# Kernel optimization log

Hardware: AMD Instinct MI355X
Metric: run time of the kernel (lower is better)

Reference implementation:

```python
import jax, jax.numpy as jnp
import numpy as np

B, SQ, SK = 2, 2048, 2048
D, H = 1024, 16
HD = D // H              # head_dim = 64
R = 128                  # rel_pos_max_distance
P = 2 * R + 1            # num_pos_ids = 257
RADIUS = 256             # local_attention_radius


def setup_inputs() -> dict:
    key = jax.random.key(0)
    ks = jax.random.split(key, 8)
    s = 0.02
    return {
        "Q": jax.random.normal(ks[0], (B, SQ, D), dtype=jnp.float32),
        "K": jax.random.normal(ks[1], (B, SK, D), dtype=jnp.float32),
        "V": jax.random.normal(ks[2], (B, SK, D), dtype=jnp.float32),
        "Wq": jax.random.normal(ks[3], (D, D), dtype=jnp.float32) * s,
        "Wk": jax.random.normal(ks[4], (D, D), dtype=jnp.float32) * s,
        "Wv": jax.random.normal(ks[5], (D, D), dtype=jnp.float32) * s,
        "Wo": jax.random.normal(ks[6], (D, D), dtype=jnp.float32) * s,
        "E": jax.random.normal(ks[7], (P, D), dtype=jnp.float32) * s,  # rel_embeds
    }


def _split_heads(x, W):
    # bias-free projection then split: B x S x D -> B x H x S x HD
    y = x @ W.T
    b, s, _ = y.shape
    return y.reshape(b, s, H, HD).transpose(0, 2, 1, 3)


def reference(Q, K, V, Wq, Wk, Wv, Wo, E):
    q = _split_heads(Q, Wq)  # B,H,Sq,HD
    k = _split_heads(K, Wk)  # B,H,Sk,HD
    v = _split_heads(V, Wv)  # B,H,Sk,HD

    # rel_embeds reshape matches torch: E[p] viewed as (head_dim, num_heads)
    rel = E.reshape(P, HD, H).transpose(2, 0, 1)           # H,P,HD
    Q_rel = jnp.einsum("bhqd,hpd->bhqp", q, rel)           # B,H,Sq,P

    # slided relative position ids: clip(j - i, -R, R) + R
    i = jnp.arange(SQ)[:, None]
    j = jnp.arange(SK)[None, :]
    rel_ids = jnp.clip(j - i, -R, R) + R                   # Sq,Sk
    rel_shift = jnp.take_along_axis(
        Q_rel, jnp.broadcast_to(rel_ids, (B, H, SQ, SK)), axis=3
    )                                                       # B,H,Sq,Sk

    energy = (jnp.einsum("bhqd,bhkd->bhqk", q, k) + rel_shift) / jnp.sqrt(
        jnp.float32(HD)
    )

    # local attention mask: True = masked (outside window of radius RADIUS)
    mask = jnp.abs(j - i) > RADIUS                          # Sq,Sk
    mask = mask & ~jnp.all(mask, axis=-1, keepdims=True)    # never mask full rows
    energy = jnp.where(mask[None, None], -jnp.inf, energy)

    attn = jax.nn.softmax(energy, axis=-1)                  # B,H,Sq,Sk
    out = jnp.einsum("bhqk,bhkd->bhqd", attn, v)            # B,H,Sq,HD
    # torch: view(B,H,Sq,HD).permute(0,2,3,1).flatten(2,3) -> B,Sq,(HD*H)
    out = out.transpose(0, 2, 3, 1).reshape(B, SQ, D)
    return out @ Wo.T
```

## Files before the change

kernel.cpp:

```cpp
#include <hip/hip_runtime.h>
#include <hip/hip_bf16.h>

#define BATCH 2
#define SQn 2048
#define SKn 2048
#define DMODEL 1024
#define NH 16
#define HD 64
#define NPOS 257
#define RWIN 128
#define RADIUS 256

typedef __attribute__((ext_vector_type(8))) short bf16x8;
typedef __attribute__((ext_vector_type(4))) float f32x4;

static __device__ __forceinline__ unsigned short f2bf(float f) {
    union { float f; unsigned u; } v; v.f = f;
    unsigned r = (v.u + 0x7FFFu + ((v.u >> 16) & 1u)) >> 16;
    return (unsigned short)r;
}
static __device__ __forceinline__ float bf2f(unsigned short b) {
    union { unsigned u; float f; } v; v.u = ((unsigned)b) << 16;
    return v.f;
}

static __device__ __forceinline__ void gl_lds16(const unsigned short* g, unsigned short* l) {
    __builtin_amdgcn_global_load_lds(
        (const __attribute__((address_space(1))) unsigned*)g,
        (__attribute__((address_space(3))) unsigned*)l, 16, 0, 0);
}

#define SWZ(row) (((row) ^ ((row) >> 2)) & 3)

__global__ __launch_bounds__(256) void convert_kernel(
    const float* __restrict__ Q, const float* __restrict__ K, const float* __restrict__ V,
    const float* __restrict__ Wq, const float* __restrict__ Wk, const float* __restrict__ Wv,
    const float* __restrict__ Wo,
    unsigned short* __restrict__ xb,
    unsigned short* __restrict__ wb,
    unsigned short* __restrict__ wob)
{
    int i = blockIdx.x * 256 + threadIdx.x;
    const float* src;
    unsigned short* dst;
    int off;
    if (i < 3145728) {
        int which = i >> 20;
        off = i & 1048575;
        src = which == 0 ? Q : (which == 1 ? K : V);
        dst = xb + (size_t)which * 4194304;
    } else {
        int i2 = i - 3145728;
        int which = i2 >> 18;
        off = i2 & 262143;
        src = which == 0 ? Wq : (which == 1 ? Wk : (which == 2 ? Wv : Wo));
        dst = which < 3 ? wb + (size_t)which * 1048576 : wob;
    }
    float4 v4 = ((const float4*)src)[off];
    ushort4 o4;
    o4.x = f2bf(v4.x); o4.y = f2bf(v4.y); o4.z = f2bf(v4.z); o4.w = f2bf(v4.w);
    ((ushort4*)dst)[off] = o4;
}

__global__ __launch_bounds__(256) void mfma_gemm(
    const unsigned short* __restrict__ Xall,
    const unsigned short* __restrict__ Wall,
    unsigned short* __restrict__ Yall)
{
    __shared__ unsigned short sA[128 * 32];
    __shared__ unsigned short sB[128 * 32];
    __shared__ unsigned short sT[64 * 136];

    const int tid  = threadIdx.x;
    const int wv   = tid >> 6;
    const int lane = tid & 63;
    const int quad = lane >> 4;
    const int l15  = lane & 15;
    const int z    = blockIdx.z;
    const int m0   = blockIdx.x * 128;
    const int n0   = blockIdx.y * 128;
    const int wr   = (wv >> 1) * 64;
    const int wc   = (wv & 1) * 64;

    const unsigned short* X = Xall + (size_t)z * (4096 * 1024);
    const unsigned short* W = Wall + (size_t)z * (1024 * 1024);

    int aoff[4], boff[4];
#pragma unroll
    for (int t = 0; t < 4; ++t) {
        int row = wr + t * 16 + l15;
        aoff[t] = row * 32 + ((quad ^ SWZ(row)) * 8);
        int col = wc + t * 16 + l15;
        boff[t] = col * 32 + ((quad ^ SWZ(col)) * 8);
    }

    int srow[2], scg[2], sf[2];
#pragma unroll
    for (int r = 0; r < 2; ++r) {
        int f = r * 256 + tid;
        sf[r] = f;
        srow[r] = f >> 2;
        scg[r] = (f & 3) ^ SWZ(srow[r]);
    }

    f32x4 acc[4][4];
#pragma unroll
    for (int i = 0; i < 4; ++i)
#pragma unroll
        for (int j = 0; j < 4; ++j)
            acc[i][j] = (f32x4){0.f, 0.f, 0.f, 0.f};

    for (int k0 = 0; k0 < 1024; k0 += 32) {
        __syncthreads();
#pragma unroll
        for (int r = 0; r < 2; ++r) {
            gl_lds16(X + (size_t)(m0 + srow[r]) * 1024 + k0 + scg[r] * 8, &sA[sf[r] * 8]);
            gl_lds16(W + (size_t)(n0 + srow[r]) * 1024 + k0 + scg[r] * 8, &sB[sf[r] * 8]);
        }
        __syncthreads();

        bf16x8 af[4], bfr[4];
#pragma unroll
        for (int t = 0; t < 4; ++t) af[t]  = *(const bf16x8*)&sA[aoff[t]];
#pragma unroll
        for (int t = 0; t < 4; ++t) bfr[t] = *(const bf16x8*)&sB[boff[t]];
#pragma unroll
        for (int i = 0; i < 4; ++i)
#pragma unroll
            for (int j = 0; j < 4; ++j)
                acc[i][j] = __builtin_amdgcn_mfma_f32_16x16x32_bf16(af[i], bfr[j], acc[i][j], 0, 0, 0);
    }

    unsigned short* Y = Yall + (size_t)z * (4096 * 1024);
    const int b_ = m0 >> 11;
    const int s0 = m0 & (SQn - 1);

    if (z < 2) {
#pragma unroll
        for (int i = 0; i < 4; ++i) {
            int mbase = s0 + wr + i * 16 + quad * 4;
#pragma unroll
            for (int j = 0; j < 4; ++j) {
                int col = n0 + wc + j * 16 + l15;
                int h = col >> 6, dd = col & 63;
                unsigned short* yb = Y + (((size_t)(b_ * NH + h) * SQn) << 6) + dd;
#pragma unroll
                for (int r = 0; r < 4; ++r)
                    yb[(size_t)(mbase + r) << 6] = f2bf(acc[i][j][r]);
            }
        }
    } else {
#pragma unroll
        for (int hh = 0; hh < 2; ++hh) {
            __syncthreads();
            if ((wv & 1) == hh) {
#pragma unroll
                for (int i = 0; i < 4; ++i) {
                    int mloc = wr + i * 16 + quad * 4;
#pragma unroll
                    for (int j = 0; j < 4; ++j) {
                        ushort4 pk;
                        pk.x = f2bf(acc[i][j][0]);
                        pk.y = f2bf(acc[i][j][1]);
                        pk.z = f2bf(acc[i][j][2]);
                        pk.w = f2bf(acc[i][j][3]);
                        *(ushort4*)&sT[(j * 16 + l15) * 136 + mloc] = pk;
                    }
                }
            }
            __syncthreads();
            int h = (n0 >> 6) + hh;
            unsigned short* yb = Y + ((size_t)(b_ * NH + h) * HD) * SKn + s0;
#pragma unroll
            for (int it = 0; it < 4; ++it) {
                int u = it * 256 + tid;
                int dd = u >> 4, mc = u & 15;
                uint4 val = *(const uint4*)&sT[dd * 136 + mc * 8];
                *(uint4*)(yb + (size_t)dd * SKn + mc * 8) = val;
            }
        }
    }
}

__global__ __launch_bounds__(256) void gemm_out(
    const unsigned short* __restrict__ X,
    const unsigned short* __restrict__ W,
    float* __restrict__ Y)
{
    __shared__ unsigned short sA[64 * 32];
    __shared__ unsigned short sB[128 * 32];

    const int tid  = threadIdx.x;
    const int wv   = tid >> 6;
    const int lane = tid & 63;
    const int quad = lane >> 4;
    const int l15  = lane & 15;
    const int m0   = blockIdx.x * 64;
    const int n0   = blockIdx.y * 128;
    const int wr   = (wv >> 1) * 32;
    const int wc   = (wv & 1) * 64;

    int aoff[2], boff[4];
#pragma unroll
    for (int i = 0; i < 2; ++i) {
        int row = wr + i * 16 + l15;
        aoff[i] = row * 32 + ((quad ^ SWZ(row)) * 8);
    }
#pragma unroll
    for (int j = 0; j < 4; ++j) {
        int col = wc + j * 16 + l15;
        boff[j] = col * 32 + ((quad ^ SWZ(col)) * 8);
    }

    const int af_  = tid;
    const int arow = af_ >> 2;
    const int acs  = (af_ & 3) ^ SWZ(arow);
    int bf_[2], brow[2], bcs[2];
#pragma unroll
    for (int r = 0; r < 2; ++r) {
        int f = r * 256 + tid;
        bf_[r] = f; brow[r] = f >> 2; bcs[r] = (f & 3) ^ SWZ(brow[r]);
    }

    f32x4 acc[2][4];
#pragma unroll
    for (int i = 0; i < 2; ++i)
#pragma unroll
        for (int j = 0; j < 4; ++j)
            acc[i][j] = (f32x4){0.f, 0.f, 0.f, 0.f};

    for (int k0 = 0; k0 < 1024; k0 += 32) {
        __syncthreads();
        gl_lds16(X + (size_t)(m0 + arow) * 1024 + k0 + acs * 8, &sA[af_ * 8]);
#pragma unroll
        for (int r = 0; r < 2; ++r)
            gl_lds16(W + (size_t)(n0 + brow[r]) * 1024 + k0 + bcs[r] * 8, &sB[bf_[r] * 8]);
        __syncthreads();

        bf16x8 af[2], bfr[4];
#pragma unroll
        for (int i = 0; i < 2; ++i) af[i]  = *(const bf16x8*)&sA[aoff[i]];
#pragma unroll
        for (int j = 0; j < 4; ++j) bfr[j] = *(const bf16x8*)&sB[boff[j]];
#pragma unroll
        for (int i = 0; i < 2; ++i)
#pragma unroll
            for (int j = 0; j < 4; ++j)
                acc[i][j] = __builtin_amdgcn_mfma_f32_16x16x32_bf16(af[i], bfr[j], acc[i][j], 0, 0, 0);
    }

#pragma unroll
    for (int i = 0; i < 2; ++i) {
        int mbase = m0 + wr + i * 16 + quad * 4;
#pragma unroll
        for (int j = 0; j < 4; ++j) {
            int col = n0 + wc + j * 16 + l15;
#pragma unroll
            for (int r = 0; r < 4; ++r)
                Y[(size_t)(mbase + r) * DMODEL + col] = acc[i][j][r];
        }
    }
}

__global__ __launch_bounds__(256) void relt_kernel(
    const float* __restrict__ E, unsigned short* __restrict__ relTb)
{
    int idx = blockIdx.x * 256 + threadIdx.x;
    const int total = NH * NPOS * HD;
    if (idx < total) {
        int d = idx & (HD - 1);
        int p = (idx >> 6) % NPOS;
        int h = idx / (NPOS * HD);
        relTb[idx] = f2bf(E[(size_t)p * DMODEL + d * NH + h]);
    }
}

#define BIAS_S 9.765625e-4f

__global__ __launch_bounds__(256) void attn_mfma(
    const unsigned short* __restrict__ q,
    const unsigned short* __restrict__ k,
    const unsigned short* __restrict__ vT,
    const unsigned short* __restrict__ relTb,
    unsigned short* __restrict__ aob)
{
    __shared__ unsigned short sQ[64 * 64];
    __shared__ unsigned short sK[64 * 64];
    __shared__ unsigned short sVt[64 * 64];
    __shared__ unsigned short sP[4][16 * 72];
    __shared__ signed char    sq8[64 * 260];

    const int tid  = threadIdx.x;
    const int w    = tid >> 6;
    const int lane = tid & 63;
    const int quad = lane >> 4;
    const int l15  = lane & 15;
    const int bh   = blockIdx.x >> 5;
    const int q0   = (blockIdx.x & 31) << 6;
    const int h    = bh & (NH - 1);
    const int b    = bh >> 4;

    {
        const unsigned short* gq = q + ((size_t)bh * SQn + q0) * HD;
#pragma unroll
        for (int r2 = 0; r2 < 2; ++r2) {
            int f = r2 * 256 + tid;
            int row = f >> 3, c = (f & 7) ^ (row & 7);
            gl_lds16(gq + row * HD + c * 8, &sQ[f * 8]);
        }
    }
    __syncthreads();

    const int qrow = w * 16 + l15;
    const int qs = (quad ^ (qrow & 7)) * 8;
    bf16x8 a0 = *(const bf16x8*)&sQ[qrow * 64 + qs];
    bf16x8 a1 = *(const bf16x8*)&sQ[qrow * 64 + (qs ^ 32)];

    const int myrow = w * 16 + quad * 4;
    for (int c5 = 0; c5 < 5; ++c5) {
        __syncthreads();
        const unsigned short* gr = relTb + ((size_t)h * NPOS + c5 * 64) * HD;
#pragma unroll
        for (int r2 = 0; r2 < 2; ++r2) {
            int f = r2 * 256 + tid;
            int row = f >> 3, c = (f & 7) ^ (row & 7);
            gl_lds16(gr + row * HD + c * 8, &sK[f * 8]);
        }
        __syncthreads();
#pragma unroll
        for (int t = 0; t < 4; ++t) {
            int prow = t * 16 + l15;
            int ks = (quad ^ (prow & 7)) * 8;
            bf16x8 b0 = *(const bf16x8*)&sK[prow * 64 + ks];
            bf16x8 b1 = *(const bf16x8*)&sK[prow * 64 + (ks ^ 32)];
            f32x4 cc = {0.f, 0.f, 0.f, 0.f};
            cc = __builtin_amdgcn_mfma_f32_16x16x32_bf16(a0, b0, cc, 0, 0, 0);
            cc = __builtin_amdgcn_mfma_f32_16x16x32_bf16(a1, b1, cc, 0, 0, 0);
            int pos = c5 * 64 + t * 16 + l15;
            if (pos < NPOS) {
#pragma unroll
                for (int r = 0; r < 4; ++r) {
                    int iq = (int)rintf(cc[r] * 128.0f);
                    iq = iq < -127 ? -127 : (iq > 127 ? 127 : iq);
                    sq8[(myrow + r) * 260 + pos] = (signed char)iq;
                }
            }
        }
    }
    __syncthreads();

    float bias0[4], bias256[4];
#pragma unroll
    for (int r = 0; r < 4; ++r) {
        bias0[r]   = (float)sq8[(myrow + r) * 260 + 0]   * BIAS_S;
        bias256[r] = (float)sq8[(myrow + r) * 260 + 256] * BIAS_S;
    }

    const int lo = (q0 - RADIUS) > 0 ? (q0 - RADIUS) : 0;
    const int hi = (q0 + 63 + RADIUS) < (SKn - 1) ? (q0 + 63 + RADIUS) : (SKn - 1);
    const int nt = ((hi - lo) >> 6) + 1;
    const int e_ = l15 - quad * 4;

    const unsigned short* kg = k  + (size_t)bh * SKn * HD;
    const unsigned short* vg = vT + (size_t)bh * HD * SKn;

    float lacc[4] = {0.f, 0.f, 0.f, 0.f};
    f32x4 o[4];
#pragma unroll
    for (int t = 0; t < 4; ++t) o[t] = (f32x4){0.f, 0.f, 0.f, 0.f};

    for (int kt = 0; kt < nt; ++kt) {
        const int kb = lo + (kt << 6);
        __syncthreads();
#pragma unroll
        for (int r2 = 0; r2 < 2; ++r2) {
            int f = r2 * 256 + tid;
            int row = f >> 3, c = (f & 7) ^ (row & 7);
            gl_lds16(kg + (size_t)(kb + row) * HD + c * 8, &sK[f * 8]);
            gl_lds16(vg + (size_t)row * SKn + kb + c * 8, &sVt[f * 8]);
        }
        __syncthreads();

        const int dtbase = kb - q0 - w * 16;
#pragma unroll
        for (int t = 0; t < 4; ++t) {
            const int dt = dtbase + t * 16;
            const int spb = (quad * 4) * 72 + t * 16 + l15;
            if (dt <= -272 || dt >= 272) {
#pragma unroll
                for (int r = 0; r < 4; ++r) sP[w][spb + r * 72] = 0;
            } else {
                int prow = t * 16 + l15;
                int ks = (quad ^ (prow & 7)) * 8;
                bf16x8 kb0 = *(const bf16x8*)&sK[prow * 64 + ks];
                bf16x8 kb1 = *(const bf16x8*)&sK[prow * 64 + (ks ^ 32)];
                f32x4 sc = {0.f, 0.f, 0.f, 0.f};
                sc = __builtin_amdgcn_mfma_f32_16x16x32_bf16(a0, kb0, sc, 0, 0, 0);
                sc = __builtin_amdgcn_mfma_f32_16x16x32_bf16(a1, kb1, sc, 0, 0, 0);

                float pv[4];
                if (dt >= -112 && dt <= 112) {
                    int idx0 = myrow * 260 + dt + 128 + e_;
#pragma unroll
                    for (int r = 0; r < 4; ++r) {
                        float bf = (float)sq8[idx0 + r * 259] * BIAS_S;
                        pv[r] = __expf(fmaf(sc[r], 0.125f, bf));
                    }
                } else if (dt >= -240 && dt <= -144) {
#pragma unroll
                    for (int r = 0; r < 4; ++r)
                        pv[r] = __expf(fmaf(sc[r], 0.125f, bias0[r]));
                } else if (dt >= 144 && dt <= 240) {
#pragma unroll
                    for (int r = 0; r < 4; ++r)
                        pv[r] = __expf(fmaf(sc[r], 0.125f, bias256[r]));
                } else {
#pragma unroll
                    for (int r = 0; r < 4; ++r) {
                        int d = dt + e_ - r;
                        bool in = (unsigned)(d + RADIUS) <= 2u * RADIUS;
                        int p = d < -RWIN ? 0 : (d > RWIN ? 2 * RWIN : d + RWIN);
                        float bf = (float)sq8[(myrow + r) * 260 + p] * BIAS_S;
                        float e = __expf(fmaf(sc[r], 0.125f, bf));
                        pv[r] = in ? e : 0.0f;
                    }
                }
#pragma unroll
                for (int r = 0; r < 4; ++r) {
                    unsigned short pb = f2bf(pv[r]);
                    sP[w][spb + r * 72] = pb;
                    lacc[r] += bf2f(pb);
                }
            }
        }

        bf16x8 p0 = *(const bf16x8*)&sP[w][l15 * 72 + quad * 8];
        bf16x8 p1 = *(const bf16x8*)&sP[w][l15 * 72 + 32 + quad * 8];
#pragma unroll
        for (int t = 0; t < 4; ++t) {
            int vrow = t * 16 + l15;
            int vs = (quad ^ (vrow & 7)) * 8;
            bf16x8 bv0 = *(const bf16x8*)&sVt[vrow * 64 + vs];
            bf16x8 bv1 = *(const bf16x8*)&sVt[vrow * 64 + (vs ^ 32)];
            o[t] = __builtin_amdgcn_mfma_f32_16x16x32_bf16(p0, bv0, o[t], 0, 0, 0);
            o[t] = __builtin_amdgcn_mfma_f32_16x16x32_bf16(p1, bv1, o[t], 0, 0, 0);
        }
    }

    float linv[4];
#pragma unroll
    for (int r = 0; r < 4; ++r) {
        float l = lacc[r];
#pragma unroll
        for (int off = 1; off <= 8; off <<= 1) l += __shfl_xor(l, off);
        linv[r] = 1.0f / l;
    }

#pragma unroll
    for (int t = 0; t < 4; ++t) {
#pragma unroll
        for (int r = 0; r < 4; ++r) {
            int i = q0 + w * 16 + quad * 4 + r;
            int c = (t * 16 + l15) * NH + h;
            aob[((size_t)b * SQn + i) * DMODEL + c] = f2bf(o[t][r] * linv[r]);
        }
    }
}

extern "C" void kernel_launch(void* const* d_in, const int* in_sizes, int n_in,
                              void* d_out, int out_size, void* d_ws, size_t ws_size,
                              hipStream_t stream) {
    const float* Q  = (const float*)d_in[0];
    const float* K  = (const float*)d_in[1];
    const float* V  = (const float*)d_in[2];
    const float* Wq = (const float*)d_in[3];
    const float* Wk = (const float*)d_in[4];
    const float* Wv = (const float*)d_in[5];
    const float* Wo = (const float*)d_in[6];
    const float* E  = (const float*)d_in[7];
    float* out = (float*)d_out;

    char* p = (char*)d_ws;
    unsigned short* xb    = (unsigned short*)p; p += (size_t)24 << 20;
    unsigned short* wb    = (unsigned short*)p; p += (size_t)6  << 20;
    unsigned short* wob   = (unsigned short*)p; p += (size_t)2  << 20;
    unsigned short* head  = (unsigned short*)p; p += (size_t)24 << 20;
    unsigned short* relTb = (unsigned short*)p; p += (size_t)1  << 20;
    unsigned short* aob   = (unsigned short*)p;

    unsigned short* qb  = head;
    unsigned short* kb  = head + 4194304;
    unsigned short* vTb = head + 8388608;

    dim3 bb(256);
    convert_kernel<<<dim3(16384), bb, 0, stream>>>(Q, K, V, Wq, Wk, Wv, Wo, xb, wb, wob);
    relt_kernel<<<dim3(1028), bb, 0, stream>>>(E, relTb);
    mfma_gemm<<<dim3(32, 8, 3), bb, 0, stream>>>(xb, wb, head);
    attn_mfma<<<dim3(BATCH * NH * (SQn / 64)), bb, 0, stream>>>(qb, kb, vTb, relTb, aob);
    gemm_out<<<dim3(64, 8), bb, 0, stream>>>(aob, wob, out);
}
```

Measured before the change: 218.3 us.

## Prefetch next K/V tile into LDS while computing from register fragments

The attention loop now loads the current K and V tile fragments from LDS into registers, synchronises, and then issues the global-to-LDS loads for the next tile, so memory fetch overlaps the MFMA and softmax work. Block indices are also remapped so that each XCD handles a contiguous group of batch-heads, which is meant to improve L2 locality of K/V reads. The cost is extra register pressure from holding 16 bf16x8 fragments per thread, which may lower occupancy. LDS still uses a single buffer, so the barrier per tile remains.

```diff
diff --git a/kernel.cpp b/kernel.cpp
--- a/kernel.cpp
+++ b/kernel.cpp
@@ -295,19 +295,22 @@
     const int lane = tid & 63;
     const int quad = lane >> 4;
     const int l15  = lane & 15;
-    const int bh   = blockIdx.x >> 5;
-    const int q0   = (blockIdx.x & 31) << 6;
+    const int xcd  = blockIdx.x & 7;
+    const int sidx = blockIdx.x >> 3;
+    const int bh   = (xcd << 2) | (sidx >> 5);
+    const int q0   = (sidx & 31) << 6;
     const int h    = bh & (NH - 1);
     const int b    = bh >> 4;
 
+    const int f1 = tid,       row1 = f1 >> 3;
+    const int c1 = ((f1 & 7) ^ (row1 & 7)) * 8;
+    const int f2 = 256 + tid, row2 = f2 >> 3;
+    const int c2 = ((f2 & 7) ^ (row2 & 7)) * 8;
+
     {
         const unsigned short* gq = q + ((size_t)bh * SQn + q0) * HD;
-#pragma unroll
-        for (int r2 = 0; r2 < 2; ++r2) {
-            int f = r2 * 256 + tid;
-            int row = f >> 3, c = (f & 7) ^ (row & 7);
-            gl_lds16(gq + row * HD + c * 8, &sQ[f * 8]);
-        }
+        gl_lds16(gq + row1 * HD + c1, &sQ[f1 * 8]);
+        gl_lds16(gq + row2 * HD + c2, &sQ[f2 * 8]);
     }
     __syncthreads();
 
@@ -320,12 +323,8 @@
     for (int c5 = 0; c5 < 5; ++c5) {
         __syncthreads();
         const unsigned short* gr = relTb + ((size_t)h * NPOS + c5 * 64) * HD;
-#pragma unroll
-        for (int r2 = 0; r2 < 2; ++r2) {
-            int f = r2 * 256 + tid;
-            int row = f >> 3, c = (f & 7) ^ (row & 7);
-            gl_lds16(gr + row * HD + c * 8, &sK[f * 8]);
-        }
+        gl_lds16(gr + row1 * HD + c1, &sK[f1 * 8]);
+        gl_lds16(gr + row2 * HD + c2, &sK[f2 * 8]);
         __syncthreads();
 #pragma unroll
         for (int t = 0; t < 4; ++t) {
@@ -369,17 +368,36 @@
 #pragma unroll
     for (int t = 0; t < 4; ++t) o[t] = (f32x4){0.f, 0.f, 0.f, 0.f};
 
+    {
+        gl_lds16(kg + (size_t)(lo + row1) * HD + c1, &sK[f1 * 8]);
+        gl_lds16(kg + (size_t)(lo + row2) * HD + c2, &sK[f2 * 8]);
+        gl_lds16(vg + (size_t)row1 * SKn + lo + c1, &sVt[f1 * 8]);
+        gl_lds16(vg + (size_t)row2 * SKn + lo + c2, &sVt[f2 * 8]);
+    }
+
     for (int kt = 0; kt < nt; ++kt) {
         const int kb = lo + (kt << 6);
         __syncthreads();
-#pragma unroll
-        for (int r2 = 0; r2 < 2; ++r2) {
-            int f = r2 * 256 + tid;
-            int row = f >> 3, c = (f & 7) ^ (row & 7);
-            gl_lds16(kg + (size_t)(kb + row) * HD + c * 8, &sK[f * 8]);
-            gl_lds16(vg + (size_t)row * SKn + kb + c * 8, &sVt[f * 8]);
-        }
-        __syncthreads();
+
+        bf16x8 kf0[4], kf1[4], vf0[4], vf1[4];
+#pragma unroll
+        for (int t = 0; t < 4; ++t) {
+            int prow = t * 16 + l15;
+            int ks = (quad ^ (prow & 7)) * 8;
+            kf0[t] = *(const bf16x8*)&sK[prow * 64 + ks];
+            kf1[t] = *(const bf16x8*)&sK[prow * 64 + (ks ^ 32)];
+            vf0[t] = *(const bf16x8*)&sVt[prow * 64 + ks];
+            vf1[t] = *(const bf16x8*)&sVt[prow * 64 + (ks ^ 32)];
+        }
+        __syncthreads();
+
+        if (kt + 1 < nt) {
+            const int kb2 = kb + 64;
+            gl_lds16(kg + (size_t)(kb2 + row1) * HD + c1, &sK[f1 * 8]);
+            gl_lds16(kg + (size_t)(kb2 + row2) * HD + c2, &sK[f2 * 8]);
+            gl_lds16(vg + (size_t)row1 * SKn + kb2 + c1, &sVt[f1 * 8]);
+            gl_lds16(vg + (size_t)row2 * SKn + kb2 + c2, &sVt[f2 * 8]);
+        }
 
         const int dtbase = kb - q0 - w * 16;
 #pragma unroll
@@ -390,13 +408,9 @@
 #pragma unroll
                 for (int r = 0; r < 4; ++r) sP[w][spb + r * 72] = 0;
             } else {
-                int prow = t * 16 + l15;
-                int ks = (quad ^ (prow & 7)) * 8;
-                bf16x8 kb0 = *(const bf16x8*)&sK[prow * 64 + ks];
-                bf16x8 kb1 = *(const bf16x8*)&sK[prow * 64 + (ks ^ 32)];
                 f32x4 sc = {0.f, 0.f, 0.f, 0.f};
-                sc = __builtin_amdgcn_mfma_f32_16x16x32_bf16(a0, kb0, sc, 0, 0, 0);
-                sc = __builtin_amdgcn_mfma_f32_16x16x32_bf16(a1, kb1, sc, 0, 0, 0);
+                sc = __builtin_amdgcn_mfma_f32_16x16x32_bf16(a0, kf0[t], sc, 0, 0, 0);
+                sc = __builtin_amdgcn_mfma_f32_16x16x32_bf16(a1, kf1[t], sc, 0, 0, 0);
 
                 float pv[4];
                 if (dt >= -112 && dt <= 112) {
@@ -438,12 +452,8 @@
         bf16x8 p1 = *(const bf16x8*)&sP[w][l15 * 72 + 32 + quad * 8];
 #pragma unroll
         for (int t = 0; t < 4; ++t) {
-            int vrow = t * 16 + l15;
-            int vs = (quad ^ (vrow & 7)) * 8;
-            bf16x8 bv0 = *(const bf16x8*)&sVt[vrow * 64 + vs];
-            bf16x8 bv1 = *(const bf16x8*)&sVt[vrow * 64 + (vs ^ 32)];
-            o[t] = __builtin_amdgcn_mfma_f32_16x16x32_bf16(p0, bv0, o[t], 0, 0, 0);
-            o[t] = __builtin_amdgcn_mfma_f32_16x16x32_bf16(p1, bv1, o[t], 0, 0, 0);
+            o[t] = __builtin_amdgcn_mfma_f32_16x16x32_bf16(p0, vf0[t], o[t], 0, 0, 0);
+            o[t] = __builtin_amdgcn_mfma_f32_16x16x32_bf16(p1, vf1[t], o[t], 0, 0, 0);
         }
     }
 
```

Result: slower. 226.5 us (+3.7%).
